# Optimization experiments

Hardware: AMD Instinct MI355X
Metric: run time of the kernel (lower is better)

Reference implementation:

```python
import jax, jax.numpy as jnp
import numpy as np

MB, NK, DM, DT = 4096, 8, 1024, 128
EPS = 1e-3  # LayerNormalization eps, added to sigma OUTSIDE sqrt


def setup_inputs() -> dict:
    key = jax.random.key(0)
    ks = jax.random.split(key, 7)
    xav = lambda fan_in, fan_out: (2.0 / (fan_in + fan_out)) ** 0.5
    return {
        "q": jax.random.normal(ks[0], (MB, NK, DM), jnp.float32),
        "k": jax.random.normal(ks[1], (MB, NK, DM), jnp.float32),
        "v": jax.random.normal(ks[2], (MB, NK, DM), jnp.float32),
        "w_qs": jax.random.normal(ks[3], (NK, DM, DT), jnp.float32) * xav(DM, DT),
        "w_ks": jax.random.normal(ks[4], (NK, DM, DT), jnp.float32) * xav(DM, DT),
        "w_vs": jax.random.normal(ks[5], (NK, DM, DT), jnp.float32) * xav(DM, DT),
        # torch Linear: weight [out, in] = [NK*DM, NK*DT]
        "proj_w": jax.random.normal(ks[6], (NK * DM, NK * DT), jnp.float32) * xav(NK * DT, NK * DM),
        "proj_b": jnp.zeros((NK * DM,), jnp.float32),
        "gamma": jnp.ones((DM,), jnp.float32),
        "beta": jnp.zeros((DM,), jnp.float32),
    }


def reference(q, k, v, w_qs, w_ks, w_vs, proj_w, proj_b, gamma, beta):
    mb, nk, dm = q.shape
    dt = w_qs.shape[-1]
    residual = v

    # torch: q.view(n_kernel, mb, d_model) on contiguous [mb, nk, dm] == raw reshape
    q_s = jnp.einsum('nbd,ndt->nbt', q.reshape(nk, mb, dm), w_qs)  # [nk, mb, dt]
    k_s = jnp.einsum('nbd,ndt->nbt', k.reshape(nk, mb, dm), w_ks)
    v_s = jnp.einsum('nbd,ndt->nbt', v.reshape(nk, mb, dm), w_vs)

    # ScaledDotProductAttention on [nk*mb, 1, dt] -> scores [.,1,1]; softmax over
    # a singleton dim is identically 1, so output == v_s (faithful to source).
    temper = np.float32(np.sqrt(dm))
    scores = jnp.sum(q_s * k_s, axis=-1) / temper            # [nk, mb]
    attn = jax.nn.softmax(scores[:, :, None, None], axis=-1)  # [nk, mb, 1, 1] == 1.0
    out = attn[..., 0] * v_s                                  # [nk, mb, dt]
    attns = attn.reshape(nk * mb, 1, 1)

    # torch .view(mb, nk*dt) on the [nk, mb, dt]-contiguous buffer (raw reshape)
    outputs = out.reshape(mb, nk * dt)
    outputs = outputs @ proj_w.T + proj_b                     # [mb, nk*dm]
    z = outputs.reshape(mb, nk, dm) + residual

    # custom LayerNormalization: unbiased std, eps outside sqrt
    mu = jnp.mean(z, axis=-1, keepdims=True)
    sigma = jnp.std(z, axis=-1, keepdims=True, ddof=1)
    output = (z - mu) / (sigma + EPS) * gamma + beta
    return (output, attns)
```

## Files before the change

### kernel.cpp

```cpp
#include <hip/hip_runtime.h>
#include <cstdint>
#include <cstddef>

#define MB_   4096
#define NK_   8
#define DM_   1024
#define DT_   128

typedef __bf16 bf16;
typedef __bf16 bf16x8 __attribute__((ext_vector_type(8)));
typedef __bf16 bf16x4 __attribute__((ext_vector_type(4)));
typedef float  f32x4  __attribute__((ext_vector_type(4)));

__device__ __forceinline__ void gload_lds16(const void* g, void* l) {
  __builtin_amdgcn_global_load_lds(
      (__attribute__((address_space(1))) void*)g,
      (__attribute__((address_space(3))) void*)l,
      16, 0, 0);
}

__device__ __forceinline__ int hsw(int r) { return (r ^ (r >> 2)) & 3; }

__global__ void prep_pw_kernel(const float* __restrict__ pw, bf16* __restrict__ pwb) {
  size_t i = ((size_t)blockIdx.x * 256 + threadIdx.x) * 4;
  float4 f = *(const float4*)&pw[i];
  bf16x4 o = { (bf16)f.x, (bf16)f.y, (bf16)f.z, (bf16)f.w };
  *(bf16x4*)&pwb[i] = o;
}

__global__ void prep_wvt_kernel(const float* __restrict__ wvs, bf16* __restrict__ wvt) {
  int o = blockIdx.x * 256 + threadIdx.x;
  int d = o & 1023;
  int t = (o >> 10) & 127;
  int n = o >> 17;
  wvt[o] = (bf16)wvs[(size_t)n * 131072 + (size_t)d * 128 + t];
}

__global__ void fill_attns_kernel(float* __restrict__ out) {
  out[(size_t)33554432 + blockIdx.x * 256 + threadIdx.x] = 1.0f;
}

__global__ __launch_bounds__(256, 2) void gemm1_kernel(
    const float* __restrict__ vflat, const bf16* __restrict__ WvT,
    bf16* __restrict__ A2)
{
  __shared__ __align__(16) bf16 As[64 * 32];
  __shared__ __align__(16) bf16 Bs[128 * 32];
  const int tid  = threadIdx.x;
  const int wave = tid >> 6, lane = tid & 63;
  const int wm = wave >> 1, wn = wave & 1;
  const int n  = blockIdx.y;
  const int b0 = blockIdx.x * 64;

  const int r  = tid >> 2;
  const int hr = hsw(r);
  const int cs = (tid & 3) ^ hr;

  const float* ag = vflat + ((size_t)(n * MB_ + b0 + r)) * 1024 + (tid & 3) * 8;
  bf16* awr = As + r * 32 + cs * 8;
  const bf16* bg = WvT + (size_t)n * 131072 + (size_t)r * 1024 + cs * 8;
  char* bsb = (char*)Bs + wave * 1024;

  f32x4 acc[2][4] = {};
  const int krow = lane & 15;
  const int cch  = lane >> 4;
  const int swoff = ((cch ^ hsw(krow)) << 4);

  for (int kt = 0; kt < 32; ++kt) {
    const bf16* bptr = bg + kt * 32;
    gload_lds16(bptr,             bsb);
    gload_lds16(bptr + 64 * 1024, bsb + 4096);
    const float* aptr = ag + kt * 32;
    float4 f0 = *(const float4*)(aptr + 0);
    float4 f1 = *(const float4*)(aptr + 4);
    bf16x8 h0 = { (bf16)f0.x, (bf16)f0.y, (bf16)f0.z, (bf16)f0.w,
                  (bf16)f1.x, (bf16)f1.y, (bf16)f1.z, (bf16)f1.w };
    *(bf16x8*)awr = h0;
    __syncthreads();

    bf16x8 af[2], bfr[4];
    #pragma unroll
    for (int i = 0; i < 2; ++i)
      af[i] = *(const bf16x8*)((const char*)As + (wm * 32 + i * 16 + krow) * 64 + swoff);
    #pragma unroll
    for (int j = 0; j < 4; ++j)
      bfr[j] = *(const bf16x8*)((const char*)Bs + (wn * 64 + j * 16 + krow) * 64 + swoff);
    #pragma unroll
    for (int i = 0; i < 2; ++i)
      #pragma unroll
      for (int j = 0; j < 4; ++j)
        acc[i][j] = __builtin_amdgcn_mfma_f32_16x16x32_bf16(af[i], bfr[j], acc[i][j], 0, 0, 0);
    __syncthreads();
  }

  #pragma unroll
  for (int i = 0; i < 2; ++i) {
    #pragma unroll
    for (int j = 0; j < 4; ++j) {
      int t = wn * 64 + j * 16 + (lane & 15);
      #pragma unroll
      for (int rr = 0; rr < 4; ++rr) {
        int b = b0 + wm * 32 + i * 16 + (lane >> 4) * 4 + rr;
        size_t off = ((size_t)(n * 512 + (b >> 3))) * 1024 + (size_t)(b & 7) * 128 + t;
        A2[off] = (bf16)acc[i][j][rr];
      }
    }
  }
}

template<bool ZB>
__global__ __launch_bounds__(512, 2) void gemm2p_kernel(
    const bf16* __restrict__ A2, const bf16* __restrict__ PW,
    const float* __restrict__ vres, const float* __restrict__ pb,
    void* __restrict__ xoutp, float2* __restrict__ stats)
{
  __shared__ __align__(16) bf16 As[4][8192];
  __shared__ __align__(16) bf16 Bs[4][8192];

  const int tid  = threadIdx.x;
  const int w    = tid >> 6;
  const int lane = tid & 63;
  const int wm   = w >> 2;
  const int wn   = w & 3;

  const int bid   = blockIdx.x;
  const int x     = bid & 7;
  const int local = bid >> 3;
  const int mt    = local & 15;
  const int nt    = x * 4 + (local >> 4);
  const int m0    = mt * 256;
  const int n0    = nt * 256;

  const int rS = tid >> 2;
  const int cS = (tid & 3) ^ hsw(rS);
  const char* aG0 = (const char*)A2 + (size_t)(m0 + rS) * 2048 + cS * 16;
  const char* aG1 = aG0 + (size_t)128 * 2048;
  const char* bG0 = (const char*)PW + (size_t)(n0 + rS) * 2048 + cS * 16;
  const char* bG1 = bG0 + (size_t)128 * 2048;

  #define STAGE_A(t) { char* d = (char*)As[(t) & 3] + tid * 16;            \
                       gload_lds16(aG0 + (t) * 64, d);                      \
                       gload_lds16(aG1 + (t) * 64, d + 8192); }
  #define STAGE_B(t) { char* d = (char*)Bs[(t) & 3] + tid * 16;            \
                       gload_lds16(bG0 + (t) * 64, d);                      \
                       gload_lds16(bG1 + (t) * 64, d + 8192); }

  STAGE_A(0); STAGE_B(0); STAGE_A(1); STAGE_B(1); STAGE_A(2); STAGE_B(2);
  asm volatile("s_waitcnt vmcnt(8)" ::: "memory");
  __builtin_amdgcn_sched_barrier(0);
  __builtin_amdgcn_s_barrier();

  f32x4 acc[8][4] = {};
  const int fr = lane & 15;
  const int g  = lane >> 4;
  const int swoff = ((g ^ hsw(fr)) << 4);
  const int aRd = (wm * 128 + fr) * 64 + swoff;
  const int bRd = (wn * 64  + fr) * 64 + swoff;

  #pragma unroll 4
  for (int t = 0; t < 32; ++t) {
    const char* pA = (const char*)As[t & 3] + aRd;
    const char* pB = (const char*)Bs[t & 3] + bRd;

    bf16x8 a[4], b[4];
    #pragma unroll
    for (int m = 0; m < 4; ++m) a[m] = *(const bf16x8*)(pA + m * 1024);
    #pragma unroll
    for (int n = 0; n < 4; ++n) b[n] = *(const bf16x8*)(pB + n * 1024);
    if (t < 29) STAGE_A(t + 3);
    __builtin_amdgcn_s_barrier();
    __builtin_amdgcn_s_setprio(1);
    #pragma unroll
    for (int m = 0; m < 4; ++m)
      #pragma unroll
      for (int n = 0; n < 4; ++n)
        acc[m][n] = __builtin_amdgcn_mfma_f32_16x16x32_bf16(a[m], b[n], acc[m][n], 0, 0, 0);
    __builtin_amdgcn_s_setprio(0);
    __builtin_amdgcn_s_barrier();

    bf16x8 a2[4];
    #pragma unroll
    for (int m = 0; m < 4; ++m) a2[m] = *(const bf16x8*)(pA + (4 + m) * 1024);
    if (t < 29) STAGE_B(t + 3);
    __builtin_amdgcn_s_barrier();
    __builtin_amdgcn_s_setprio(1);
    #pragma unroll
    for (int m = 0; m < 4; ++m)
      #pragma unroll
      for (int n = 0; n < 4; ++n)
        acc[4 + m][n] = __builtin_amdgcn_mfma_f32_16x16x32_bf16(a2[m], b[n], acc[4 + m][n], 0, 0, 0);
    __builtin_amdgcn_s_setprio(0);
    if (t < 29)       { asm volatile("s_waitcnt vmcnt(8)" ::: "memory"); }
    else if (t == 29) { asm volatile("s_waitcnt vmcnt(4)" ::: "memory"); }
    else if (t == 30) { asm volatile("s_waitcnt vmcnt(0)" ::: "memory"); }
    __builtin_amdgcn_sched_barrier(0);
    __builtin_amdgcn_s_barrier();
  }
  #undef STAGE_A
  #undef STAGE_B

  float pbv[4];
  #pragma unroll
  for (int n = 0; n < 4; ++n) pbv[n] = pb[n0 + wn * 64 + n * 16 + fr];

  float sthr[8][4], qthr[8][4];
  #pragma unroll
  for (int m = 0; m < 8; ++m) {
    #pragma unroll
    for (int r = 0; r < 4; ++r) {
      int lrow = wm * 128 + m * 16 + g * 4 + r;
      const float* vrow = vres + (size_t)(m0 + lrow) * 8192 + n0 + wn * 64 + fr;
      float s = 0.0f, q2 = 0.0f;
      #pragma unroll
      for (int n = 0; n < 4; ++n) {
        float xv = acc[m][n][r] + pbv[n] + vrow[n * 16];
        acc[m][n][r] = xv;
        s += xv; q2 += xv * xv;
      }
      sthr[m][r] = s; qthr[m][r] = q2;
    }
  }
  #pragma unroll
  for (int m = 0; m < 8; ++m) {
    #pragma unroll
    for (int n = 0; n < 4; ++n) {
      size_t coff = (size_t)(n0 + wn * 64 + n * 16 + fr);
      #pragma unroll
      for (int r = 0; r < 4; ++r) {
        size_t off = (size_t)(m0 + wm * 128 + m * 16 + g * 4 + r) * 8192 + coff;
        if (ZB) ((bf16*)xoutp)[off] = (bf16)acc[m][n][r];
        else    ((float*)xoutp)[off] = acc[m][n][r];
      }
    }
  }
  #pragma unroll
  for (int m = 0; m < 8; ++m)
    #pragma unroll
    for (int r = 0; r < 4; ++r) {
      float s = sthr[m][r], q2 = qthr[m][r];
      #pragma unroll
      for (int msk = 8; msk >= 1; msk >>= 1) {
        s  += __shfl_xor(s,  msk, 64);
        q2 += __shfl_xor(q2, msk, 64);
      }
      sthr[m][r] = s; qthr[m][r] = q2;
    }
  float* sredS = (float*)&As[0][0];
  float* sredQ = sredS + 1024;
  if (fr == 0) {
    #pragma unroll
    for (int m = 0; m < 8; ++m)
      #pragma unroll
      for (int r = 0; r < 4; ++r) {
        int lrow = wm * 128 + m * 16 + g * 4 + r;
        sredS[lrow * 4 + wn] = sthr[m][r];
        sredQ[lrow * 4 + wn] = qthr[m][r];
      }
  }
  __syncthreads();
  if (tid < 256) {
    float S  = sredS[tid * 4] + sredS[tid * 4 + 1] + sredS[tid * 4 + 2] + sredS[tid * 4 + 3];
    float SS = sredQ[tid * 4] + sredQ[tid * 4 + 1] + sredQ[tid * 4 + 2] + sredQ[tid * 4 + 3];
    int rid = (m0 + tid) * 8 + (nt >> 2);
    stats[(size_t)rid * 4 + (nt & 3)] = make_float2(S, SS);
  }
}

template<bool ZB>
__global__ __launch_bounds__(256) void ln_apply_kernel(
    const void* xin, const float2* __restrict__ stats,
    const float* __restrict__ gamma, const float* __restrict__ beta,
    float* outp)
{
  const int bid = blockIdx.x;
  const int tid = threadIdx.x;
  float2 st0 = stats[(size_t)bid * 4 + 0];
  float2 st1 = stats[(size_t)bid * 4 + 1];
  float2 st2 = stats[(size_t)bid * 4 + 2];
  float2 st3 = stats[(size_t)bid * 4 + 3];
  float S  = st0.x + st1.x + st2.x + st3.x;
  float SS = st0.y + st1.y + st2.y + st3.y;
  float mu  = S * (1.0f / 1024.0f);
  float var = (SS - 1024.0f * mu * mu) * (1.0f / 1023.0f);
  var = var < 0.0f ? 0.0f : var;
  float rs = 1.0f / (sqrtf(var) + 1e-3f);

  const size_t base = (size_t)bid * 1024 + tid * 4;
  float4 xv;
  if (ZB) {
    bf16x4 xb = *(const bf16x4*)((const bf16*)xin + base);
    xv.x = (float)xb[0]; xv.y = (float)xb[1]; xv.z = (float)xb[2]; xv.w = (float)xb[3];
  } else {
    xv = *(const float4*)((const float*)xin + base);
  }
  float4 ga = *(const float4*)&gamma[tid * 4];
  float4 be = *(const float4*)&beta[tid * 4];
  float4 y;
  y.x = (xv.x - mu) * rs * ga.x + be.x;
  y.y = (xv.y - mu) * rs * ga.y + be.y;
  y.z = (xv.z - mu) * rs * ga.z + be.z;
  y.w = (xv.w - mu) * rs * ga.w + be.w;
  *(float4*)&outp[base] = y;
}

extern "C" void kernel_launch(void* const* d_in, const int* in_sizes, int n_in,
                              void* d_out, int out_size, void* d_ws, size_t ws_size,
                              hipStream_t stream) {
  const float* v     = (const float*)d_in[2];
  const float* wvs   = (const float*)d_in[5];
  const float* pw    = (const float*)d_in[6];
  const float* pb    = (const float*)d_in[7];
  const float* gamma = (const float*)d_in[8];
  const float* beta  = (const float*)d_in[9];
  float* out = (float*)d_out;

  const size_t OFF_WVT = 16777216;
  const size_t OFF_A2  = OFF_WVT + 2097152;
  const size_t OFF_ST  = OFF_A2 + 8388608;
  const size_t OFF_X   = OFF_ST + 1048576;
  const size_t NEED_ZB = OFF_X + 67108864;

  bf16*   PWb   = (bf16*)d_ws;
  bf16*   WvT   = (bf16*)((char*)d_ws + OFF_WVT);
  bf16*   A2    = (bf16*)((char*)d_ws + OFF_A2);
  float2* stats = (float2*)((char*)d_ws + OFF_ST);
  const bool zb = (ws_size >= NEED_ZB);
  void* xbuf = zb ? (void*)((char*)d_ws + OFF_X) : (void*)out;

  hipLaunchKernelGGL(prep_pw_kernel,    dim3(8192), dim3(256), 0, stream, pw, PWb);
  hipLaunchKernelGGL(prep_wvt_kernel,   dim3(4096), dim3(256), 0, stream, wvs, WvT);
  hipLaunchKernelGGL(fill_attns_kernel, dim3(128),  dim3(256), 0, stream, out);
  hipLaunchKernelGGL(gemm1_kernel, dim3(64, 8), dim3(256), 0, stream, v, WvT, A2);
  if (zb) {
    hipLaunchKernelGGL((gemm2p_kernel<true>),  dim3(512), dim3(512), 0, stream,
                       A2, PWb, v, pb, xbuf, stats);
    hipLaunchKernelGGL((ln_apply_kernel<true>),  dim3(32768), dim3(256), 0, stream,
                       xbuf, stats, gamma, beta, out);
  } else {
    hipLaunchKernelGGL((gemm2p_kernel<false>), dim3(512), dim3(512), 0, stream,
                       A2, PWb, v, pb, xbuf, stats);
    hipLaunchKernelGGL((ln_apply_kernel<false>), dim3(32768), dim3(256), 0, stream,
                       xbuf, stats, gamma, beta, out);
  }
}
```

Before: 214.6 us.

## Merge prep kernels, shorten GEMM2 prefetch depth, fuse epilogue loops and attns fill

Folds the two weight-conversion kernels into one launch and moves the attns=1 fill into the layer-norm apply kernel, which removes two kernel launches. The GEMM2 LDS pipeline now prefetches two stages ahead instead of three, which lowers the number of outstanding loads and may expose more memory latency. The epilogue is restructured so each row's residual add, store, shuffle reduction and LDS partial write happen in one pass, instead of keeping per-thread sum arrays across separate loops. This is meant to cut register pressure.

```diff
diff --git a/kernel.cpp b/kernel.cpp
--- a/kernel.cpp
+++ b/kernel.cpp
@@ -21,23 +21,21 @@
 
 __device__ __forceinline__ int hsw(int r) { return (r ^ (r >> 2)) & 3; }
 
-__global__ void prep_pw_kernel(const float* __restrict__ pw, bf16* __restrict__ pwb) {
-  size_t i = ((size_t)blockIdx.x * 256 + threadIdx.x) * 4;
-  float4 f = *(const float4*)&pw[i];
-  bf16x4 o = { (bf16)f.x, (bf16)f.y, (bf16)f.z, (bf16)f.w };
-  *(bf16x4*)&pwb[i] = o;
-}
-
-__global__ void prep_wvt_kernel(const float* __restrict__ wvs, bf16* __restrict__ wvt) {
-  int o = blockIdx.x * 256 + threadIdx.x;
-  int d = o & 1023;
-  int t = (o >> 10) & 127;
-  int n = o >> 17;
-  wvt[o] = (bf16)wvs[(size_t)n * 131072 + (size_t)d * 128 + t];
-}
-
-__global__ void fill_attns_kernel(float* __restrict__ out) {
-  out[(size_t)33554432 + blockIdx.x * 256 + threadIdx.x] = 1.0f;
+__global__ void prep_kernel(const float* __restrict__ pw, bf16* __restrict__ pwb,
+                            const float* __restrict__ wvs, bf16* __restrict__ wvt) {
+  int b = blockIdx.x;
+  if (b < 8192) {
+    size_t i = ((size_t)b * 256 + threadIdx.x) * 4;
+    float4 f = *(const float4*)&pw[i];
+    bf16x4 o = { (bf16)f.x, (bf16)f.y, (bf16)f.z, (bf16)f.w };
+    *(bf16x4*)&pwb[i] = o;
+  } else {
+    int o = (b - 8192) * 256 + threadIdx.x;
+    int d = o & 1023;
+    int t = (o >> 10) & 127;
+    int n = o >> 17;
+    wvt[o] = (bf16)wvs[(size_t)n * 131072 + (size_t)d * 128 + t];
+  }
 }
 
 __global__ __launch_bounds__(256, 2) void gemm1_kernel(
@@ -109,7 +107,7 @@
 }
 
 template<bool ZB>
-__global__ __launch_bounds__(512, 2) void gemm2p_kernel(
+__global__ __launch_bounds__(512, 2) void gemm2pv_kernel(
     const bf16* __restrict__ A2, const bf16* __restrict__ PW,
     const float* __restrict__ vres, const float* __restrict__ pb,
     void* __restrict__ xoutp, float2* __restrict__ stats)
@@ -145,8 +143,8 @@
                        gload_lds16(bG0 + (t) * 64, d);                      \
                        gload_lds16(bG1 + (t) * 64, d + 8192); }
 
-  STAGE_A(0); STAGE_B(0); STAGE_A(1); STAGE_B(1); STAGE_A(2); STAGE_B(2);
-  asm volatile("s_waitcnt vmcnt(8)" ::: "memory");
+  STAGE_A(0); STAGE_B(0); STAGE_A(1); STAGE_B(1);
+  asm volatile("s_waitcnt vmcnt(4)" ::: "memory");
   __builtin_amdgcn_sched_barrier(0);
   __builtin_amdgcn_s_barrier();
 
@@ -167,7 +165,7 @@
     for (int m = 0; m < 4; ++m) a[m] = *(const bf16x8*)(pA + m * 1024);
     #pragma unroll
     for (int n = 0; n < 4; ++n) b[n] = *(const bf16x8*)(pB + n * 1024);
-    if (t < 29) STAGE_A(t + 3);
+    if (t < 30) STAGE_A(t + 2);
     __builtin_amdgcn_s_barrier();
     __builtin_amdgcn_s_setprio(1);
     #pragma unroll
@@ -181,7 +179,7 @@
     bf16x8 a2[4];
     #pragma unroll
     for (int m = 0; m < 4; ++m) a2[m] = *(const bf16x8*)(pA + (4 + m) * 1024);
-    if (t < 29) STAGE_B(t + 3);
+    if (t < 30) STAGE_B(t + 2);
     __builtin_amdgcn_s_barrier();
     __builtin_amdgcn_s_setprio(1);
     #pragma unroll
@@ -190,8 +188,7 @@
       for (int n = 0; n < 4; ++n)
         acc[4 + m][n] = __builtin_amdgcn_mfma_f32_16x16x32_bf16(a2[m], b[n], acc[4 + m][n], 0, 0, 0);
     __builtin_amdgcn_s_setprio(0);
-    if (t < 29)       { asm volatile("s_waitcnt vmcnt(8)" ::: "memory"); }
-    else if (t == 29) { asm volatile("s_waitcnt vmcnt(4)" ::: "memory"); }
+    if (t < 30)       { asm volatile("s_waitcnt vmcnt(4)" ::: "memory"); }
     else if (t == 30) { asm volatile("s_waitcnt vmcnt(0)" ::: "memory"); }
     __builtin_amdgcn_sched_barrier(0);
     __builtin_amdgcn_s_barrier();
@@ -203,66 +200,47 @@
   #pragma unroll
   for (int n = 0; n < 4; ++n) pbv[n] = pb[n0 + wn * 64 + n * 16 + fr];
 
-  float sthr[8][4], qthr[8][4];
+  float* sredS = (float*)&As[0][0];
+  float* sredQ = sredS + 1024;
+
+  const float* vb0 = vres + (size_t)(m0 + wm * 128 + g * 4) * 8192 + (n0 + wn * 64 + fr);
+
   #pragma unroll
   for (int m = 0; m < 8; ++m) {
     #pragma unroll
     for (int r = 0; r < 4; ++r) {
-      int lrow = wm * 128 + m * 16 + g * 4 + r;
-      const float* vrow = vres + (size_t)(m0 + lrow) * 8192 + n0 + wn * 64 + fr;
+      const float* vrow = vb0 + (size_t)(m * 16 + r) * 8192;
+      float xv[4];
       float s = 0.0f, q2 = 0.0f;
       #pragma unroll
       for (int n = 0; n < 4; ++n) {
-        float xv = acc[m][n][r] + pbv[n] + vrow[n * 16];
-        acc[m][n][r] = xv;
-        s += xv; q2 += xv * xv;
-      }
-      sthr[m][r] = s; qthr[m][r] = q2;
-    }
-  }
-  #pragma unroll
-  for (int m = 0; m < 8; ++m) {
-    #pragma unroll
-    for (int n = 0; n < 4; ++n) {
-      size_t coff = (size_t)(n0 + wn * 64 + n * 16 + fr);
-      #pragma unroll
-      for (int r = 0; r < 4; ++r) {
-        size_t off = (size_t)(m0 + wm * 128 + m * 16 + g * 4 + r) * 8192 + coff;
-        if (ZB) ((bf16*)xoutp)[off] = (bf16)acc[m][n][r];
-        else    ((float*)xoutp)[off] = acc[m][n][r];
-      }
-    }
-  }
-  #pragma unroll
-  for (int m = 0; m < 8; ++m)
-    #pragma unroll
-    for (int r = 0; r < 4; ++r) {
-      float s = sthr[m][r], q2 = qthr[m][r];
+        xv[n] = acc[m][n][r] + pbv[n] + vrow[n * 16];
+        s += xv[n]; q2 += xv[n] * xv[n];
+      }
+      size_t ro = (size_t)(m0 + wm * 128 + m * 16 + g * 4 + r) * 8192 + (n0 + wn * 64 + fr);
+      #pragma unroll
+      for (int n = 0; n < 4; ++n) {
+        if (ZB) ((bf16*)xoutp)[ro + n * 16] = (bf16)xv[n];
+        else    ((float*)xoutp)[ro + n * 16] = xv[n];
+      }
       #pragma unroll
       for (int msk = 8; msk >= 1; msk >>= 1) {
         s  += __shfl_xor(s,  msk, 64);
         q2 += __shfl_xor(q2, msk, 64);
       }
-      sthr[m][r] = s; qthr[m][r] = q2;
+      if (fr == 0) {
+        int lrow = wm * 128 + m * 16 + g * 4 + r;
+        sredS[lrow * 4 + wn] = s;
+        sredQ[lrow * 4 + wn] = q2;
+      }
     }
-  float* sredS = (float*)&As[0][0];
-  float* sredQ = sredS + 1024;
-  if (fr == 0) {
-    #pragma unroll
-    for (int m = 0; m < 8; ++m)
-      #pragma unroll
-      for (int r = 0; r < 4; ++r) {
-        int lrow = wm * 128 + m * 16 + g * 4 + r;
-        sredS[lrow * 4 + wn] = sthr[m][r];
-        sredQ[lrow * 4 + wn] = qthr[m][r];
-      }
   }
   __syncthreads();
   if (tid < 256) {
     float S  = sredS[tid * 4] + sredS[tid * 4 + 1] + sredS[tid * 4 + 2] + sredS[tid * 4 + 3];
     float SS = sredQ[tid * 4] + sredQ[tid * 4 + 1] + sredQ[tid * 4 + 2] + sredQ[tid * 4 + 3];
-    int rid = (m0 + tid) * 8 + (nt >> 2);
-    stats[(size_t)rid * 4 + (nt & 3)] = make_float2(S, SS);
+    int lnrow = (m0 + tid) * 8 + (n0 >> 10);
+    stats[(size_t)lnrow * 4 + ((n0 >> 8) & 3)] = make_float2(S, SS);
   }
 }
 
@@ -274,6 +252,8 @@
 {
   const int bid = blockIdx.x;
   const int tid = threadIdx.x;
+  if (bid < 128) outp[(size_t)33554432 + bid * 256 + tid] = 1.0f;
+
   float2 st0 = stats[(size_t)bid * 4 + 0];
   float2 st1 = stats[(size_t)bid * 4 + 1];
   float2 st2 = stats[(size_t)bid * 4 + 2];
@@ -327,17 +307,15 @@
   const bool zb = (ws_size >= NEED_ZB);
   void* xbuf = zb ? (void*)((char*)d_ws + OFF_X) : (void*)out;
 
-  hipLaunchKernelGGL(prep_pw_kernel,    dim3(8192), dim3(256), 0, stream, pw, PWb);
-  hipLaunchKernelGGL(prep_wvt_kernel,   dim3(4096), dim3(256), 0, stream, wvs, WvT);
-  hipLaunchKernelGGL(fill_attns_kernel, dim3(128),  dim3(256), 0, stream, out);
+  hipLaunchKernelGGL(prep_kernel, dim3(12288), dim3(256), 0, stream, pw, PWb, wvs, WvT);
   hipLaunchKernelGGL(gemm1_kernel, dim3(64, 8), dim3(256), 0, stream, v, WvT, A2);
   if (zb) {
-    hipLaunchKernelGGL((gemm2p_kernel<true>),  dim3(512), dim3(512), 0, stream,
+    hipLaunchKernelGGL((gemm2pv_kernel<true>),  dim3(512), dim3(512), 0, stream,
                        A2, PWb, v, pb, xbuf, stats);
-    hipLaunchKernelGGL((ln_apply_kernel<true>),  dim3(32768), dim3(256), 0, stream,
+    hipLaunchKernelGGL((ln_apply_kernel<true>), dim3(32768), dim3(256), 0, stream,
                        xbuf, stats, gamma, beta, out);
   } else {
-    hipLaunchKernelGGL((gemm2p_kernel<false>), dim3(512), dim3(512), 0, stream,
+    hipLaunchKernelGGL((gemm2pv_kernel<false>), dim3(512), dim3(512), 0, stream,
                        A2, PWb, v, pb, xbuf, stats);
     hipLaunchKernelGGL((ln_apply_kernel<false>), dim3(32768), dim3(256), 0, stream,
                        xbuf, stats, gamma, beta, out);
```

New measurement: 202.2 us. 1.06x faster.
